# Performance work log

Hardware: AMD Instinct MI355X
Metric: run time of the kernel (lower is better)

## Reference

```python
import jax, jax.numpy as jnp
import numpy as np

C_IN = 1024
C_INTER = 512
EPS = 1e-5
STD = 0.01


def _conv1x1(x, w, b):
    # x: [B,C,H,W], w: [O,C] (1x1 conv kernel squeezed), b: [O]
    return jnp.einsum('bchw,oc->bohw', x, w) + b[None, :, None, None]


def setup_inputs() -> dict:
    key = jax.random.key(0)
    ks = jax.random.split(key, 12)
    def w(k, o, i):
        return jax.random.normal(k, (o, i), jnp.float32) * STD
    def b(k, o):
        return jax.random.normal(k, (o,), jnp.float32) * STD
    return {
        'x': jax.random.normal(ks[0], (8, C_IN, 64, 64), jnp.float32),
        'theta_w': w(ks[1], C_INTER, C_IN), 'theta_b': b(ks[2], C_INTER),
        'phi_w': w(ks[3], C_INTER, C_IN), 'phi_b': b(ks[4], C_INTER),
        'g_w': w(ks[5], C_INTER, C_IN), 'g_b': b(ks[6], C_INTER),
        'wz_w': w(ks[7], C_IN, C_INTER), 'wz_b': b(ks[8], C_IN),
        'bn_gamma': jax.random.normal(ks[9], (C_IN,), jnp.float32) * 0.1,
        'bn_beta': jax.random.normal(ks[10], (C_IN,), jnp.float32) * 0.1,
    }


def reference(x, theta_w, theta_b, phi_w, phi_b, g_w, g_b, wz_w, wz_b, bn_gamma, bn_beta):
    B, C, H, W = x.shape
    # theta on full-res input: [B, Ci, H*W]
    theta = _conv1x1(x, theta_w, theta_b).reshape(B, C_INTER, H * W)
    # 2x2 stride-2 max pool for phi/g path
    xp = jax.lax.reduce_window(x, -jnp.inf, jax.lax.max,
                               (1, 1, 2, 2), (1, 1, 2, 2), 'VALID')
    Hp, Wp = xp.shape[2], xp.shape[3]
    phi = _conv1x1(xp, phi_w, phi_b).reshape(B, C_INTER, Hp * Wp)
    g = _conv1x1(xp, g_w, g_b).reshape(B, C_INTER, Hp * Wp)
    # attention: [B, H*W, Hp*Wp], scaled softmax
    attn = jnp.einsum('bcn,bcm->bnm', theta, phi) * (C_INTER ** -0.5)
    attn = jax.nn.softmax(attn, axis=-1)
    # aggregate: [B, Ci, H*W]
    y = jnp.einsum('bcm,bnm->bcn', g, attn).reshape(B, C_INTER, H, W)
    z = _conv1x1(y, wz_w, wz_b)
    # BatchNorm2d (training-mode batch stats, biased var)
    mean = z.mean(axis=(0, 2, 3), keepdims=True)
    var = jnp.mean((z - mean) ** 2, axis=(0, 2, 3), keepdims=True)
    z = (z - mean) * jax.lax.rsqrt(var + EPS)
    z = z * bn_gamma[None, :, None, None] + bn_beta[None, :, None, None]
    return x + z
```

## Files before the change

kernel.cpp:

```cpp
#include <hip/hip_runtime.h>

typedef unsigned short u16;
typedef unsigned int u32;
typedef __attribute__((ext_vector_type(8))) short bf16x8;
typedef __attribute__((ext_vector_type(4))) float f32x4;

__device__ __forceinline__ u16 f2bf(float f) {
  u32 u = __builtin_bit_cast(u32, f);
  u = u + 0x7FFFu + ((u >> 16) & 1u);
  return (u16)(u >> 16);
}
__device__ __forceinline__ float bf2f(u16 s) {
  return __builtin_bit_cast(float, (u32)s << 16);
}

__device__ __forceinline__ void gload_lds16(const u16* g, u16* l) {
  __builtin_amdgcn_global_load_lds(
      (const __attribute__((address_space(1))) u32*)g,
      (__attribute__((address_space(3))) u32*)l, 16, 0, 0);
}

__global__ __launch_bounds__(256) void k_cvt4(
    const float* __restrict__ s0, const float* __restrict__ s1,
    const float* __restrict__ s2, const float* __restrict__ s3,
    u16* __restrict__ d0, u16* __restrict__ d1, u16* __restrict__ d2,
    u16* __restrict__ d3) {
  int gid = blockIdx.x * 256 + threadIdx.x;
  int which = gid >> 17;
  int loc = (gid & 131071) * 4;
  const float* s = which == 0 ? s0 : which == 1 ? s1 : which == 2 ? s2 : s3;
  u16* d = which == 0 ? d0 : which == 1 ? d1 : which == 2 ? d2 : d3;
  float4 v = *(const float4*)(s + loc);
  u32 lo = (u32)f2bf(v.x) | ((u32)f2bf(v.y) << 16);
  u32 hi = (u32)f2bf(v.z) | ((u32)f2bf(v.w) << 16);
  uint2 o; o.x = lo; o.y = hi;
  *(uint2*)(d + loc) = o;
}

__global__ __launch_bounds__(256) void k_transpose_pool(
    const float* __restrict__ x, u16* __restrict__ xT, u16* __restrict__ xpT) {
  __shared__ u16 lds[128 * 64];
  const int t = threadIdx.x;
  const int c0 = blockIdx.x * 64;
  const int by = blockIdx.y;
  const int b = blockIdx.z;

  {
    const int nf = (t & 31) * 4;
    const int swz = 8 * (t & 7);
    const float* xb =
        x + ((size_t)(b * 1024 + c0 + (t >> 5)) * 4096) + by * 128 + nf;
#pragma unroll
    for (int u = 0; u < 8; ++u) {
      const int c_l = (t >> 5) + 8 * u;
      float4 v = *(const float4*)(xb + (size_t)(8 * u) * 4096);
      const int col = c_l ^ swz;
      lds[(nf + 0) * 64 + col] = f2bf(v.x);
      lds[(nf + 1) * 64 + col] = f2bf(v.y);
      lds[(nf + 2) * 64 + col] = f2bf(v.z);
      lds[(nf + 3) * 64 + col] = f2bf(v.w);
    }
  }
  __syncthreads();
  {
#pragma unroll
    for (int v = 0; v < 4; ++v) {
      const int idx = t + 256 * v;
      const int n_l = idx >> 3;
      const int cb = (idx & 7) * 8;
      const int col = cb ^ (8 * ((n_l >> 2) & 7));
      bf16x8 d = *(const bf16x8*)&lds[n_l * 64 + col];
      *(bf16x8*)&xT[((size_t)b * 4096 + by * 128 + n_l) * 1024 + c0 + cb] = d;
    }
  }
  {
    const int m_w = t >> 3;
    const int cb = (t & 7) * 8;
    const int na = 2 * m_w, nb = na + 1, nc = na + 64, nd = na + 65;
    bf16x8 va = *(const bf16x8*)&lds[na * 64 + (cb ^ (8 * ((na >> 2) & 7)))];
    bf16x8 vb = *(const bf16x8*)&lds[nb * 64 + (cb ^ (8 * ((nb >> 2) & 7)))];
    bf16x8 vc = *(const bf16x8*)&lds[nc * 64 + (cb ^ (8 * ((nc >> 2) & 7)))];
    bf16x8 vd = *(const bf16x8*)&lds[nd * 64 + (cb ^ (8 * ((nd >> 2) & 7)))];
    bf16x8 o;
#pragma unroll
    for (int j = 0; j < 8; ++j) {
      float m = fmaxf(fmaxf(bf2f((u16)va[j]), bf2f((u16)vb[j])),
                      fmaxf(bf2f((u16)vc[j]), bf2f((u16)vd[j])));
      o[j] = (short)f2bf(m);
    }
    *(bf16x8*)&xpT[((size_t)b * 1024 + by * 32 + m_w) * 1024 + c0 + cb] = o;
  }
}

template <int BIAS_MODE>
__global__ __launch_bounds__(256, 2) void gemm_nt(
    const u16* __restrict__ A, long aBS, const u16* __restrict__ Bm, long bBS,
    u16* __restrict__ Cm, long cBS, const float* __restrict__ bias, int N,
    int K, float scale) {
  __shared__ u16 Alds[2][128 * 32];
  __shared__ u16 Blds[2][128 * 32];
  const int t = threadIdx.x;
  const int b = blockIdx.z;
  const int bm = blockIdx.y, bn = blockIdx.x;
  const u16* Ab = A + (size_t)b * aBS + (size_t)bm * 128 * K;
  const u16* Bb = Bm + (size_t)b * bBS + (size_t)bn * 128 * K;

  const int lane = t & 63;
  const int w = t >> 6;
  const int wrow = w >> 1, wcol = w & 1;
  const int lr = lane & 15;
  const int kg = lane >> 4;

  f32x4 acc[4][4] = {};

  const int e0 = t * 8;
  const int r0 = e0 >> 5;
  const int k0i = e0 & 31;
  const int steps = K >> 5;

#define STAGE(buf, ks)                                                   \
  do {                                                                   \
    const int kb = (ks) * 32;                                            \
    gload_lds16(Ab + (size_t)r0 * K + kb + k0i, &Alds[buf][e0]);         \
    gload_lds16(Ab + (size_t)(r0 + 64) * K + kb + k0i,                   \
                &Alds[buf][e0 + 2048]);                                  \
    gload_lds16(Bb + (size_t)r0 * K + kb + k0i, &Blds[buf][e0]);         \
    gload_lds16(Bb + (size_t)(r0 + 64) * K + kb + k0i,                   \
                &Blds[buf][e0 + 2048]);                                  \
  } while (0)

  STAGE(0, 0);
  for (int ks = 0; ks < steps; ++ks) {
    const int cur = ks & 1;
    __syncthreads();
    if (ks + 1 < steps) STAGE(cur ^ 1, ks + 1);
    bf16x8 af[4], bfr[4];
#pragma unroll
    for (int i = 0; i < 4; ++i) {
      af[i] =
          *(const bf16x8*)&Alds[cur][(wrow * 64 + i * 16 + lr) * 32 + kg * 8];
      bfr[i] =
          *(const bf16x8*)&Blds[cur][(wcol * 64 + i * 16 + lr) * 32 + kg * 8];
    }
#pragma unroll
    for (int i = 0; i < 4; ++i)
#pragma unroll
      for (int j = 0; j < 4; ++j)
        acc[i][j] = __builtin_amdgcn_mfma_f32_16x16x32_bf16(af[i], bfr[j],
                                                            acc[i][j], 0, 0, 0);
  }
#undef STAGE

  u16* Cb = Cm + (size_t)b * cBS;
#pragma unroll
  for (int i = 0; i < 4; ++i) {
#pragma unroll
    for (int j = 0; j < 4; ++j) {
      int row0 = bm * 128 + wrow * 64 + i * 16 + kg * 4;
      int col = bn * 128 + wcol * 64 + j * 16 + lr;
      float bj = (BIAS_MODE == 2) ? bias[col] : 0.f;
#pragma unroll
      for (int r = 0; r < 4; ++r) {
        float v = acc[i][j][r] * scale;
        if (BIAS_MODE == 1) v += bias[row0 + r];
        if (BIAS_MODE == 2) v += bj;
        Cb[(size_t)(row0 + r) * N + col] = f2bf(v);
      }
    }
  }
}

template <int BIAS_MODE>
__global__ __launch_bounds__(512, 2) void gemm256(
    const u16* __restrict__ A, long aBS, const u16* __restrict__ Bm, long bBS,
    u16* __restrict__ Cm, long cBS, const float* __restrict__ bias, int N,
    int K, float scale) {
  __shared__ u16 ALDS[2][16384];
  __shared__ u16 BLDS[2][16384];
  const int t = threadIdx.x;
  u32 gx = gridDim.x, gy = gridDim.y;
  u32 nwg = gx * gy * gridDim.z;
  u32 wg = blockIdx.x + gx * (blockIdx.y + gy * blockIdx.z);
  u32 swz = (wg & 7) * (nwg >> 3) + (wg >> 3);
  const int bn = swz % gx;
  u32 tmp = swz / gx;
  const int bm = tmp % gy;
  const int b = tmp / gy;

  const u16* Agb = A + (size_t)b * aBS + (size_t)bm * 256 * K;
  const u16* Bgb = Bm + (size_t)b * bBS + (size_t)bn * 256 * K;

  const int lane = t & 63;
  const int wid = t >> 6;
  const int wr = wid >> 2;
  const int wc = wid & 3;
  const int lr = lane & 15;
  const int kg = (lane >> 4) & 3;
  const int T = K >> 6;

  f32x4 acc[8][4] = {};

#define STAGE_G(LDSARR, GB, h, ktn)                                          \
  if ((ktn) < T) {                                                           \
    {                                                                        \
      const int r = t >> 3;                                                  \
      gload_lds16(GB + (size_t)((h)*128 + r) * K + (size_t)(ktn)*64 +        \
                      (((t & 7) ^ (r & 7)) * 8),                             \
                  &LDSARR[(ktn) & 1][(h)*8192 + t * 8]);                     \
    }                                                                        \
    {                                                                        \
      const int idx = 512 + t;                                               \
      const int r = idx >> 3;                                                \
      gload_lds16(GB + (size_t)((h)*128 + r) * K + (size_t)(ktn)*64 +        \
                      (((t & 7) ^ (r & 7)) * 8),                             \
                  &LDSARR[(ktn) & 1][(h)*8192 + idx * 8]);                   \
    }                                                                        \
  }
#define STAGE_A(h, ktn) STAGE_G(ALDS, Agb, h, ktn)
#define STAGE_B(h, ktn) STAGE_G(BLDS, Bgb, h, ktn)

#define LDA4(mh, kk)                                                         \
  _Pragma("unroll") for (int m2 = 0; m2 < 4; ++m2) {                         \
    const int row = wr * 128 + ((mh)*4 + m2) * 16 + lr;                      \
    aF[m2] = *(const bf16x8*)&ALDS[cb][row * 64 +                            \
                                       ((((kk)*4 + kg) ^ (lr & 7)) * 8)];    \
  }
#define LDB4(kk)                                                             \
  _Pragma("unroll") for (int n = 0; n < 4; ++n) {                            \
    const int row = wc * 64 + n * 16 + lr;                                   \
    bF[n] = *(const bf16x8*)&BLDS[cb][row * 64 +                             \
                                      ((((kk)*4 + kg) ^ (lr & 7)) * 8)];     \
  }
#define MFMA16(M0)                                                           \
  __builtin_amdgcn_s_setprio(1);                                             \
  _Pragma("unroll") for (int n = 0; n < 4; ++n) {                            \
    acc[(M0) + 0][n] = __builtin_amdgcn_mfma_f32_16x16x32_bf16(              \
        aF[0], bF[n], acc[(M0) + 0][n], 0, 0, 0);                            \
    acc[(M0) + 1][n] = __builtin_amdgcn_mfma_f32_16x16x32_bf16(              \
        aF[1], bF[n], acc[(M0) + 1][n], 0, 0, 0);                            \
    acc[(M0) + 2][n] = __builtin_amdgcn_mfma_f32_16x16x32_bf16(              \
        aF[2], bF[n], acc[(M0) + 2][n], 0, 0, 0);                            \
    acc[(M0) + 3][n] = __builtin_amdgcn_mfma_f32_16x16x32_bf16(              \
        aF[3], bF[n], acc[(M0) + 3][n], 0, 0, 0);                            \
  }                                                                          \
  __builtin_amdgcn_s_setprio(0);
#define CFENCE asm volatile("" ::: "memory")

  STAGE_B(0, 0);
  STAGE_B(1, 0);
  STAGE_A(0, 0);
  STAGE_A(1, 0);
  STAGE_B(0, 1);

  for (int kt = 0; kt < T; ++kt) {
    const int cb = kt & 1;
    bf16x8 aF[4], bF[4];
    asm volatile("s_waitcnt vmcnt(2)" ::: "memory");
    __builtin_amdgcn_s_barrier();
    STAGE_B(1, kt + 1);
    LDB4(0);
    LDA4(0, 0);
    MFMA16(0);
    CFENCE;
    __builtin_amdgcn_s_barrier();
    STAGE_A(0, kt + 1);
    LDA4(1, 0);
    MFMA16(4);
    CFENCE;
    __builtin_amdgcn_s_barrier();
    STAGE_A(1, kt + 1);
    LDB4(1);
    LDA4(0, 1);
    MFMA16(0);
    CFENCE;
    __builtin_amdgcn_s_barrier();
    STAGE_B(0, kt + 2);
    LDA4(1, 1);
    MFMA16(4);
    CFENCE;
    __builtin_amdgcn_s_barrier();
  }

  u16* Cb = Cm + (size_t)b * cBS;
#pragma unroll
  for (int m = 0; m < 8; ++m) {
    const int row0 = bm * 256 + wr * 128 + m * 16 + kg * 4;
#pragma unroll
    for (int n = 0; n < 4; ++n) {
      const int col = bn * 256 + wc * 64 + n * 16 + lr;
      float bj = (BIAS_MODE == 2) ? bias[col] : 0.f;
#pragma unroll
      for (int r = 0; r < 4; ++r) {
        float v = acc[m][n][r] * scale;
        if (BIAS_MODE == 1) v += bias[row0 + r];
        if (BIAS_MODE == 2) v += bj;
        Cb[(size_t)(row0 + r) * N + col] = f2bf(v);
      }
    }
  }
#undef STAGE_G
#undef STAGE_A
#undef STAGE_B
#undef LDA4
#undef LDB4
#undef MFMA16
#undef CFENCE
}

__global__ __launch_bounds__(256) void k_softmax(u16* __restrict__ S) {
  const int t = threadIdx.x;
  const int lane = t & 63;
  const size_t row = (size_t)blockIdx.x * 4 + (t >> 6);
  u16* p = S + row * 1024 + lane * 16;
  uint4 d0 = *(const uint4*)p;
  uint4 d1 = *(const uint4*)(p + 8);
  u32 u[8] = {d0.x, d0.y, d0.z, d0.w, d1.x, d1.y, d1.z, d1.w};
  float v[16];
#pragma unroll
  for (int i = 0; i < 8; ++i) {
    v[2 * i] = bf2f((u16)(u[i] & 0xffff));
    v[2 * i + 1] = bf2f((u16)(u[i] >> 16));
  }
  float m = v[0];
#pragma unroll
  for (int i = 1; i < 16; ++i) m = fmaxf(m, v[i]);
  for (int o = 32; o > 0; o >>= 1) m = fmaxf(m, __shfl_xor(m, o));
  const float LOG2E = 1.44269504088896f;
  float s = 0.f;
#pragma unroll
  for (int i = 0; i < 16; ++i) {
    v[i] = exp2f((v[i] - m) * LOG2E);
    s += v[i];
  }
  for (int o = 32; o > 0; o >>= 1) s += __shfl_xor(s, o);
  float inv = 1.0f / s;
#pragma unroll
  for (int i = 0; i < 8; ++i)
    u[i] = (u32)f2bf(v[2 * i] * inv) | ((u32)f2bf(v[2 * i + 1] * inv) << 16);
  uint4 o0; o0.x = u[0]; o0.y = u[1]; o0.z = u[2]; o0.w = u[3];
  uint4 o1; o1.x = u[4]; o1.y = u[5]; o1.z = u[6]; o1.w = u[7];
  *(uint4*)p = o0;
  *(uint4*)(p + 8) = o1;
}

__global__ __launch_bounds__(256) void k_stats(const u16* __restrict__ z,
                                               float2* __restrict__ stats) {
  const int o = blockIdx.x;
  const int t = threadIdx.x;
  float s = 0.f, q = 0.f;
  for (int b = 0; b < 8; ++b) {
    const u16* p = z + ((size_t)b * 1024 + o) * 4096;
    for (int i = t * 4; i < 4096; i += 1024) {
      uint2 d = *(const uint2*)(p + i);
      float a0 = bf2f((u16)(d.x & 0xffff)), a1 = bf2f((u16)(d.x >> 16));
      float a2 = bf2f((u16)(d.y & 0xffff)), a3 = bf2f((u16)(d.y >> 16));
      s += a0 + a1 + a2 + a3;
      q += a0 * a0 + a1 * a1 + a2 * a2 + a3 * a3;
    }
  }
  for (int o2 = 32; o2 > 0; o2 >>= 1) {
    s += __shfl_xor(s, o2);
    q += __shfl_xor(q, o2);
  }
  __shared__ float2 red[4];
  if ((t & 63) == 0) red[t >> 6] = make_float2(s, q);
  __syncthreads();
  if (t == 0) {
    float S_ = 0.f, Q_ = 0.f;
    for (int i = 0; i < 4; ++i) { S_ += red[i].x; Q_ += red[i].y; }
    stats[o] = make_float2(S_, Q_);
  }
}

__global__ __launch_bounds__(256) void k_apply(
    const float* __restrict__ x, const u16* __restrict__ z,
    const float2* __restrict__ stats, const float* __restrict__ gamma,
    const float* __restrict__ beta, float* __restrict__ out) {
  size_t i4 = (size_t)blockIdx.x * 256 + threadIdx.x;
  size_t e = i4 * 4;
  int c = (int)((e >> 12) & 1023);
  float2 st = stats[c];
  const float cnt = 1.0f / 32768.0f;
  float mean = st.x * cnt;
  float var = st.y * cnt - mean * mean;
  float g = rsqrtf(var + 1e-5f) * gamma[c];
  float sh = beta[c] - mean * g;
  float4 xv = *(const float4*)(x + e);
  uint2 zd = *(const uint2*)(z + e);
  float z0 = bf2f((u16)(zd.x & 0xffff)), z1 = bf2f((u16)(zd.x >> 16));
  float z2 = bf2f((u16)(zd.y & 0xffff)), z3 = bf2f((u16)(zd.y >> 16));
  float4 ov;
  ov.x = xv.x + z0 * g + sh;
  ov.y = xv.y + z1 * g + sh;
  ov.z = xv.z + z2 * g + sh;
  ov.w = xv.w + z3 * g + sh;
  *(float4*)(out + e) = ov;
}

extern "C" void kernel_launch(void* const* d_in, const int* in_sizes, int n_in,
                              void* d_out, int out_size, void* d_ws,
                              size_t ws_size, hipStream_t stream) {
  const float* x = (const float*)d_in[0];
  const float* theta_w = (const float*)d_in[1];
  const float* theta_b = (const float*)d_in[2];
  const float* phi_w = (const float*)d_in[3];
  const float* phi_b = (const float*)d_in[4];
  const float* g_w = (const float*)d_in[5];
  const float* g_b = (const float*)d_in[6];
  const float* wz_w = (const float*)d_in[7];
  const float* wz_b = (const float*)d_in[8];
  const float* gamma = (const float*)d_in[9];
  const float* beta = (const float*)d_in[10];
  float* out = (float*)d_out;

  char* w = (char*)d_ws;
  const size_t MiB = (size_t)1 << 20;
  u16* WT = (u16*)(w + 0 * MiB);
  u16* WP = (u16*)(w + 1 * MiB);
  u16* WG = (u16*)(w + 2 * MiB);
  u16* WZ = (u16*)(w + 3 * MiB);
  u16* XT = (u16*)(w + 4 * MiB);
  u16* XPT = (u16*)(w + 68 * MiB);
  u16* THETA = (u16*)(w + 84 * MiB);
  u16* PHI = (u16*)(w + 116 * MiB);
  u16* G = (u16*)(w + 124 * MiB);
  u16* S = XT;
  u16* YT = (u16*)(w + 132 * MiB);
  u16* Z = S;
  float2* stats = (float2*)(w + 164 * MiB);

  k_cvt4<<<2048, 256, 0, stream>>>(theta_w, phi_w, g_w, wz_w, WT, WP, WG, WZ);
  k_transpose_pool<<<dim3(16, 32, 8), 256, 0, stream>>>(x, XT, XPT);
  gemm256<2><<<dim3(2, 128, 1), 512, 0, stream>>>(
      XT, 0, WT, 0, THETA, 0, theta_b, 512, 1024, 1.0f);
  gemm_nt<2><<<dim3(4, 8, 8), 256, 0, stream>>>(
      XPT, (long)1024 * 1024, WP, 0, PHI, (long)1024 * 512, phi_b, 512, 1024,
      1.0f);
  gemm_nt<1><<<dim3(8, 4, 8), 256, 0, stream>>>(
      WG, 0, XPT, (long)1024 * 1024, G, (long)512 * 1024, g_b, 1024, 1024,
      1.0f);
  gemm256<0><<<dim3(4, 16, 8), 512, 0, stream>>>(
      THETA, (long)4096 * 512, PHI, (long)1024 * 512, S, (long)4096 * 1024,
      nullptr, 1024, 512, 0.04419417382415922f);
  k_softmax<<<8192, 256, 0, stream>>>(S);
  gemm256<0><<<dim3(2, 16, 8), 512, 0, stream>>>(
      S, (long)4096 * 1024, G, (long)512 * 1024, YT, (long)4096 * 512, nullptr,
      512, 1024, 1.0f);
  gemm256<1><<<dim3(16, 4, 8), 512, 0, stream>>>(
      WZ, 0, YT, (long)4096 * 512, Z, (long)1024 * 4096, wz_b, 4096, 512,
      1.0f);
  k_stats<<<1024, 256, 0, stream>>>(Z, stats);
  k_apply<<<32768, 256, 0, stream>>>(x, Z, stats, gamma, beta, out);

  (void)in_sizes; (void)n_in; (void)out_size; (void)ws_size;
}
```

Measured before the change: 586.5 us.

## Merge phi/g GEMMs into one launch and front-load A staging in gemm256

Replaces the two separate gemm_nt launches for phi and g with a single gemm_dual kernel whose 512 blocks are split between the two projections, so the GPU runs both in one launch instead of two 256-block launches. In gemm256, all next-tile A and B global-to-LDS loads are now issued at the top of the k iteration rather than interleaved between barriers, and the last iteration waits for vmcnt(0). The aim is to issue prefetches earlier and cut launch overhead. The cost is a runtime bias_mode branch in the merged kernel and possibly more loads in flight at once.

```diff
diff --git a/kernel.cpp b/kernel.cpp
--- a/kernel.cpp
+++ b/kernel.cpp
@@ -92,18 +92,34 @@
   }
 }
 
-template <int BIAS_MODE>
-__global__ __launch_bounds__(256, 2) void gemm_nt(
-    const u16* __restrict__ A, long aBS, const u16* __restrict__ Bm, long bBS,
-    u16* __restrict__ Cm, long cBS, const float* __restrict__ bias, int N,
-    int K, float scale) {
+__global__ __launch_bounds__(256, 2) void gemm_dual(
+    const u16* __restrict__ XPT, const u16* __restrict__ WP,
+    const u16* __restrict__ WG, u16* __restrict__ PHI, u16* __restrict__ G,
+    const float* __restrict__ phi_b, const float* __restrict__ g_b) {
   __shared__ u16 Alds[2][128 * 32];
   __shared__ u16 Blds[2][128 * 32];
   const int t = threadIdx.x;
-  const int b = blockIdx.z;
-  const int bm = blockIdx.y, bn = blockIdx.x;
-  const u16* Ab = A + (size_t)b * aBS + (size_t)bm * 128 * K;
-  const u16* Bb = Bm + (size_t)b * bBS + (size_t)bn * 128 * K;
+  const int K = 1024;
+
+  int id = blockIdx.x;
+  const u16 *Ab, *Bb;
+  u16* Cm;
+  const float* bias;
+  int N, bias_mode, bm, bn;
+  if (id < 256) {
+    bn = id & 3; bm = (id >> 2) & 7; const int b = id >> 5;
+    Ab = XPT + (size_t)b * 1024 * 1024 + (size_t)bm * 128 * K;
+    Bb = WP + (size_t)bn * 128 * K;
+    Cm = PHI + (size_t)b * 1024 * 512;
+    bias = phi_b; N = 512; bias_mode = 2;
+  } else {
+    id -= 256;
+    bn = id & 7; bm = (id >> 3) & 3; const int b = id >> 5;
+    Ab = WG + (size_t)bm * 128 * K;
+    Bb = XPT + (size_t)b * 1024 * 1024 + (size_t)bn * 128 * K;
+    Cm = G + (size_t)b * 512 * 1024;
+    bias = g_b; N = 1024; bias_mode = 1;
+  }
 
   const int lane = t & 63;
   const int w = t >> 6;
@@ -151,20 +167,18 @@
   }
 #undef STAGE
 
-  u16* Cb = Cm + (size_t)b * cBS;
 #pragma unroll
   for (int i = 0; i < 4; ++i) {
 #pragma unroll
     for (int j = 0; j < 4; ++j) {
       int row0 = bm * 128 + wrow * 64 + i * 16 + kg * 4;
       int col = bn * 128 + wcol * 64 + j * 16 + lr;
-      float bj = (BIAS_MODE == 2) ? bias[col] : 0.f;
+      float bj = (bias_mode == 2) ? bias[col] : 0.f;
 #pragma unroll
       for (int r = 0; r < 4; ++r) {
-        float v = acc[i][j][r] * scale;
-        if (BIAS_MODE == 1) v += bias[row0 + r];
-        if (BIAS_MODE == 2) v += bj;
-        Cb[(size_t)(row0 + r) * N + col] = f2bf(v);
+        float v = acc[i][j][r];
+        v += (bias_mode == 1) ? bias[row0 + r] : bj;
+        Cm[(size_t)(row0 + r) * N + col] = f2bf(v);
       }
     }
   }
@@ -255,20 +269,24 @@
   for (int kt = 0; kt < T; ++kt) {
     const int cb = kt & 1;
     bf16x8 aF[4], bF[4];
-    asm volatile("s_waitcnt vmcnt(2)" ::: "memory");
+    if (kt + 1 < T) {
+      asm volatile("s_waitcnt vmcnt(2)" ::: "memory");
+    } else {
+      asm volatile("s_waitcnt vmcnt(0)" ::: "memory");
+    }
     __builtin_amdgcn_s_barrier();
     STAGE_B(1, kt + 1);
+    STAGE_A(0, kt + 1);
+    STAGE_A(1, kt + 1);
     LDB4(0);
     LDA4(0, 0);
     MFMA16(0);
     CFENCE;
     __builtin_amdgcn_s_barrier();
-    STAGE_A(0, kt + 1);
     LDA4(1, 0);
     MFMA16(4);
     CFENCE;
     __builtin_amdgcn_s_barrier();
-    STAGE_A(1, kt + 1);
     LDB4(1);
     LDA4(0, 1);
     MFMA16(0);
@@ -433,12 +451,7 @@
   k_transpose_pool<<<dim3(16, 32, 8), 256, 0, stream>>>(x, XT, XPT);
   gemm256<2><<<dim3(2, 128, 1), 512, 0, stream>>>(
       XT, 0, WT, 0, THETA, 0, theta_b, 512, 1024, 1.0f);
-  gemm_nt<2><<<dim3(4, 8, 8), 256, 0, stream>>>(
-      XPT, (long)1024 * 1024, WP, 0, PHI, (long)1024 * 512, phi_b, 512, 1024,
-      1.0f);
-  gemm_nt<1><<<dim3(8, 4, 8), 256, 0, stream>>>(
-      WG, 0, XPT, (long)1024 * 1024, G, (long)512 * 1024, g_b, 1024, 1024,
-      1.0f);
+  gemm_dual<<<512, 256, 0, stream>>>(XPT, WP, WG, PHI, G, phi_b, g_b);
   gemm256<0><<<dim3(4, 16, 8), 512, 0, stream>>>(
       THETA, (long)4096 * 512, PHI, (long)1024 * 512, S, (long)4096 * 1024,
       nullptr, 1024, 512, 0.04419417382415922f);
```

Result: faster. 549.1 us (-6.4%).
